# Kernel optimization log

Hardware: AMD Instinct MI355X
Metric: run time of the kernel (lower is better)

The kernel has to match this reference:

```python
import jax, jax.numpy as jnp
import numpy as np
from jax import lax

NPOINT = 1024   # num_points (FPS centroids)
RADIUS = 0.2    # ball-query radius
K = 32          # samples per ball
FILTERS = [64, 64, 128]


def setup_inputs() -> dict:
    key = jax.random.key(0)
    ks = jax.random.split(key, 10)
    B, N, C = 16, 4096, 64
    xyz = jax.random.uniform(ks[0], (B, N, 3), dtype=jnp.float32)   # unit-cube cloud
    points = jax.random.normal(ks[1], (B, N, C), dtype=jnp.float32)
    inp = {"xyz": xyz, "points": points}
    cin = C + 3  # use_xyz=True concatenates relative xyz
    for i, f in enumerate(FILTERS):
        scale = np.sqrt(2.0 / (cin + f)).astype(np.float32)  # glorot_normal
        inp[f"w{i}"] = jax.random.normal(ks[2 + i], (cin, f), dtype=jnp.float32) * scale
        inp[f"b{i}"] = jnp.zeros((f,), dtype=jnp.float32)
        cin = f
    return inp


def farthest_point_sample(xyz, npoint):
    # Serial greedy FPS. xyz: [B,N,3] -> idx [B,npoint] int32
    B, N, _ = xyz.shape

    def body(carry, _):
        dist, far = carry                                   # [B,N], [B]
        centroid = jnp.take_along_axis(xyz, far[:, None, None], axis=1)  # [B,1,3]
        d = jnp.sum((xyz - centroid) ** 2, axis=-1)         # [B,N]
        dist = jnp.minimum(dist, d)
        nxt = jnp.argmax(dist, axis=-1).astype(jnp.int32)
        return (dist, nxt), far

    init = (jnp.full((B, N), 1e10, xyz.dtype), jnp.zeros((B,), jnp.int32))
    _, idxs = lax.scan(body, init, None, length=npoint)
    return idxs.T  # [B,npoint]


def query_ball(radius, nsample, xyz, new_xyz):
    # First-nsample-in-order points within radius; pad with first hit (CUDA semantics).
    B, N, _ = xyz.shape
    d2 = jnp.sum((new_xyz[:, :, None, :] - xyz[:, None, :, :]) ** 2, axis=-1)  # [B,S,N]
    mask = d2 <= radius * radius
    order = jnp.where(mask, jnp.arange(N, dtype=jnp.int32)[None, None, :], N)
    idx_sorted = jnp.sort(order, axis=-1)[..., :nsample]    # first K valid indices
    first = idx_sorted[..., :1]
    first = jnp.where(first < N, first, 0)                  # empty-ball fallback
    return jnp.where(idx_sorted < N, idx_sorted, first)     # [B,S,K]


def reference(xyz, points, w0, b0, w1, b1, w2, b2):
    B, N, _ = xyz.shape
    fps_idx = farthest_point_sample(xyz, NPOINT)                    # [B,S]
    new_xyz = jnp.take_along_axis(xyz, fps_idx[:, :, None], axis=1)  # [B,S,3]
    idx = query_ball(RADIUS, K, xyz, new_xyz)                        # [B,S,K]

    bix = jnp.arange(B)[:, None, None]
    grouped_xyz = xyz[bix, idx] - new_xyz[:, :, None, :]             # [B,S,K,3] recentered
    grouped_pts = points[bix, idx]                                   # [B,S,K,C]
    g = jnp.concatenate([grouped_pts, grouped_xyz], axis=-1)         # [B,S,K,C+3]

    for w, b in ((w0, b0), (w1, b1), (w2, b2)):                      # shared 1x1-conv MLP
        g = jax.nn.relu(jnp.einsum('bskc,cf->bskf', g, w) + b)
    new_points = jnp.max(g, axis=2)                                  # max-pool over ball
    return new_xyz, new_points
```

## Files before the change

kernel.cpp:

```cpp
#include <hip/hip_runtime.h>
#include <stdint.h>

#define BB 16
#define NN 4096
#define CC 64
#define NPOINT 1024
#define KK 32
#define F1 64
#define F2 64
#define F3 128

#define FPS_T 512
#define PPT (NN / FPS_T)

#if defined(__has_builtin)
#if __has_builtin(__builtin_amdgcn_update_dpp)
#define HAS_DPP 1
#endif
#endif

#ifdef HAS_DPP
template <int CTRL>
__device__ __forceinline__ unsigned long long dpp_move64(unsigned long long k) {
    int lo = __builtin_amdgcn_update_dpp(0, (int)(unsigned)k,         CTRL, 0xF, 0xF, false);
    int hi = __builtin_amdgcn_update_dpp(0, (int)(unsigned)(k >> 32), CTRL, 0xF, 0xF, false);
    return ((unsigned long long)(unsigned)hi << 32) | (unsigned)lo;
}
__device__ __forceinline__ unsigned long long wave_max_key(unsigned long long key) {
    unsigned long long o;
    o = dpp_move64<0x111>(key); if (o > key) key = o;
    o = dpp_move64<0x112>(key); if (o > key) key = o;
    o = dpp_move64<0x114>(key); if (o > key) key = o;
    o = dpp_move64<0x118>(key); if (o > key) key = o;
    o = dpp_move64<0x142>(key); if (o > key) key = o;
    o = dpp_move64<0x143>(key); if (o > key) key = o;
    return key;
}
#else
__device__ __forceinline__ unsigned long long wave_max_key(unsigned long long key) {
#pragma unroll
    for (int off = 32; off > 0; off >>= 1) {
        unsigned long long o = __shfl_xor(key, off, 64);
        if (o > key) key = o;
    }
    return key;
}
#endif

#define SMEM_BYTES 83968

__global__ __launch_bounds__(512)
void fused_kernel(const float* __restrict__ xyz,
                  const float* __restrict__ points,
                  const float* __restrict__ w0, const float* __restrict__ b0,
                  const float* __restrict__ w1, const float* __restrict__ b1,
                  const float* __restrict__ w2, const float* __restrict__ b2,
                  float* __restrict__ out_xyz,
                  float* __restrict__ out_points,
                  int* __restrict__ ctr) {
    __shared__ __align__(16) char smem[SMEM_BYTES];
    const int tid = threadIdx.x;

    if (blockIdx.x < BB) {
        asm volatile("s_setprio 3");
        float* xs = (float*)smem;
        float* ys = xs + NN;
        float* zs = ys + NN;
        unsigned long long (*wred)[FPS_T / 64] =
            (unsigned long long (*)[FPS_T / 64])(smem + 49152);
        float* cbuf = (float*)(smem + 49280);

        const int b = blockIdx.x;
        const int lane = tid & 63, wid = tid >> 6;
        const float* __restrict__ xb = xyz + (size_t)b * (NN * 3);

        float px[PPT], py[PPT], pz[PPT], dist[PPT];
#pragma unroll
        for (int t = 0; t < PPT; ++t) {
            int p = tid + t * FPS_T;
            px[t] = xb[p * 3 + 0];
            py[t] = xb[p * 3 + 1];
            pz[t] = xb[p * 3 + 2];
            xs[p] = px[t]; ys[p] = py[t]; zs[p] = pz[t];
            dist[t] = 1e10f;
        }
        __syncthreads();

        float cx = xs[0], cy = ys[0], cz = zs[0];
        float* xo = out_xyz + (size_t)b * NPOINT * 3;

        for (int i = 0; i < NPOINT; ++i) {
            if (tid == 0) {
                cbuf[(i & 7) * 3 + 0] = cx;
                cbuf[(i & 7) * 3 + 1] = cy;
                cbuf[(i & 7) * 3 + 2] = cz;
            }
            float bd = -1.0f; int bp = 0;
#pragma unroll
            for (int t = 0; t < PPT; ++t) {
                float dx = __fsub_rn(px[t], cx);
                float dy = __fsub_rn(py[t], cy);
                float dz = __fsub_rn(pz[t], cz);
                float d  = __fadd_rn(__fadd_rn(__fmul_rn(dx, dx), __fmul_rn(dy, dy)),
                                     __fmul_rn(dz, dz));
                float nd = fminf(dist[t], d);
                dist[t] = nd;
                if (nd > bd) { bd = nd; bp = tid + t * FPS_T; }
            }
            unsigned long long key = (((unsigned long long)__float_as_uint(bd)) << 32)
                                   | (unsigned int)(NN - 1 - bp);
            key = wave_max_key(key);
            if (lane == 63) wred[i & 1][wid] = key;
            __syncthreads();

            unsigned long long best = wred[i & 1][0];
#pragma unroll
            for (int w = 1; w < FPS_T / 64; ++w) {
                unsigned long long o = wred[i & 1][w];
                if (o > best) best = o;
            }
            int bi = (NN - 1) - (int)(best & 0xffffffffu);

            cx = xs[bi]; cy = ys[bi]; cz = zs[bi];

            if (tid == 0 && (i & 7) == 7) {
                asm volatile("s_waitcnt vmcnt(0)" ::: "memory");
                if (i > 7)
                    __hip_atomic_store(&ctr[b * 16], i - 7,
                                       __ATOMIC_RELAXED, __HIP_MEMORY_SCOPE_AGENT);
                const unsigned* cbu = (const unsigned*)cbuf;
                unsigned* dst = (unsigned*)(xo + (size_t)(i - 7) * 3);
#pragma unroll
                for (int q = 0; q < 24; ++q)
                    __hip_atomic_store(dst + q, cbu[q],
                                       __ATOMIC_RELAXED, __HIP_MEMORY_SCOPE_AGENT);
            }
        }
        if (tid == 0) {
            asm volatile("s_waitcnt vmcnt(0)" ::: "memory");
            __hip_atomic_store(&ctr[b * 16], NPOINT,
                               __ATOMIC_RELAXED, __HIP_MEMORY_SCOPE_AGENT);
        }
    } else {
        float (*gbuf)[68] = (float (*)[68])smem;
        float (*hbuf)[F1] = (float (*)[F1])(smem + 8704);
        float (*pmax)[F3] = (float (*)[F3])(smem + 16896);
        unsigned long long* cmask = (unsigned long long*)(smem + 20992);
        int* nbr = (int*)(smem + 21504);

        const int gi = blockIdx.x - BB;
        const int s = gi >> 4;
        const int b = gi & 15;
        const int g = b * NPOINT + s;
        const int f = tid & 63;
        const int wid = tid >> 6;

        if (tid == 0) {
            while (__hip_atomic_load(&ctr[b * 16], __ATOMIC_RELAXED,
                                     __HIP_MEMORY_SCOPE_AGENT) < s + 1)
                __builtin_amdgcn_s_sleep(2);
        }
        __syncthreads();

        unsigned int ux = __hip_atomic_load((unsigned int*)&out_xyz[(size_t)g * 3 + 0],
                                            __ATOMIC_RELAXED, __HIP_MEMORY_SCOPE_AGENT);
        unsigned int uy = __hip_atomic_load((unsigned int*)&out_xyz[(size_t)g * 3 + 1],
                                            __ATOMIC_RELAXED, __HIP_MEMORY_SCOPE_AGENT);
        unsigned int uz = __hip_atomic_load((unsigned int*)&out_xyz[(size_t)g * 3 + 2],
                                            __ATOMIC_RELAXED, __HIP_MEMORY_SCOPE_AGENT);
        const float cx = __uint_as_float(ux);
        const float cy = __uint_as_float(uy);
        const float cz = __uint_as_float(uz);

        {
            const float* __restrict__ xb = xyz + (size_t)b * (NN * 3);
#pragma unroll
            for (int j = 0; j < 8; ++j) {
                int chunk = wid * 8 + j;
                int p = chunk * 64 + f;
                float x = xb[p * 3 + 0];
                float y = xb[p * 3 + 1];
                float z = xb[p * 3 + 2];
                float dx = __fsub_rn(cx, x);
                float dy = __fsub_rn(cy, y);
                float dz = __fsub_rn(cz, z);
                float d2 = __fadd_rn(__fadd_rn(__fmul_rn(dx, dx), __fmul_rn(dy, dy)),
                                     __fmul_rn(dz, dz));
                unsigned long long m = __ballot(d2 <= 0.04f);
                if (f == 0) cmask[chunk] = m;
            }
        }
        __syncthreads();

        if (tid < 64) {
            unsigned long long m = cmask[tid];
            int cnt = (int)__popcll(m);
            int v = cnt;
#pragma unroll
            for (int off = 1; off < 64; off <<= 1) {
                int u = __shfl_up(v, off, 64);
                if (tid >= off) v += u;
            }
            int excl = v - cnt;
            int total = __shfl(v, 63, 64);
            unsigned long long mm = m;
            int r = excl;
            while (mm && r < KK) {
                int bpos = __ffsll(mm) - 1;
                mm &= mm - 1;
                nbr[r++] = tid * 64 + bpos;
            }
            if (total < KK) {
                unsigned long long nz = __ballot(cnt > 0);
                int fchunk = __ffsll(nz) - 1;
                unsigned long long fm = cmask[fchunk];
                int first = fchunk * 64 + __ffsll(fm) - 1;
                if (tid >= total && tid < KK) nbr[tid] = first;
            }
        }
        __syncthreads();

        {
            const float* __restrict__ pb = points + (size_t)b * NN * CC;
#pragma unroll
            for (int m = 0; m < 4; ++m) {
                int k = wid + 8 * m;
                int idx = nbr[k] & (NN - 1);
                gbuf[k][f] = pb[(size_t)idx * CC + f];
            }
            if (tid < 96) {
                int k = tid & 31, q = tid >> 5;
                int idx = nbr[k] & (NN - 1);
                float v = xyz[((size_t)b * NN + idx) * 3 + q];
                float cq = (q == 0) ? cx : ((q == 1) ? cy : cz);
                gbuf[k][CC + q] = __fsub_rn(v, cq);
            }
        }
        __syncthreads();

        float acc[4];

#pragma unroll
        for (int m = 0; m < 4; ++m) acc[m] = 0.0f;
#pragma unroll 4
        for (int c4 = 0; c4 < 64; c4 += 4) {
            float wv0 = w0[(c4 + 0) * F1 + f];
            float wv1 = w0[(c4 + 1) * F1 + f];
            float wv2 = w0[(c4 + 2) * F1 + f];
            float wv3 = w0[(c4 + 3) * F1 + f];
#pragma unroll
            for (int m = 0; m < 4; ++m) {
                float4 gv = *(const float4*)&gbuf[wid + 8 * m][c4];
                acc[m] = fmaf(gv.x, wv0, acc[m]);
                acc[m] = fmaf(gv.y, wv1, acc[m]);
                acc[m] = fmaf(gv.z, wv2, acc[m]);
                acc[m] = fmaf(gv.w, wv3, acc[m]);
            }
        }
        {
            float wv0 = w0[64 * F1 + f];
            float wv1 = w0[65 * F1 + f];
            float wv2 = w0[66 * F1 + f];
#pragma unroll
            for (int m = 0; m < 4; ++m) {
                int k = wid + 8 * m;
                acc[m] = fmaf(gbuf[k][64], wv0, acc[m]);
                acc[m] = fmaf(gbuf[k][65], wv1, acc[m]);
                acc[m] = fmaf(gbuf[k][66], wv2, acc[m]);
            }
        }
        {
            float bb = b0[f];
#pragma unroll
            for (int m = 0; m < 4; ++m)
                hbuf[wid + 8 * m][f] = fmaxf(acc[m] + bb, 0.0f);
        }
        __syncthreads();

#pragma unroll
        for (int m = 0; m < 4; ++m) acc[m] = 0.0f;
#pragma unroll 4
        for (int c4 = 0; c4 < 64; c4 += 4) {
            float wv0 = w1[(c4 + 0) * F2 + f];
            float wv1 = w1[(c4 + 1) * F2 + f];
            float wv2 = w1[(c4 + 2) * F2 + f];
            float wv3 = w1[(c4 + 3) * F2 + f];
#pragma unroll
            for (int m = 0; m < 4; ++m) {
                float4 gv = *(const float4*)&hbuf[wid + 8 * m][c4];
                acc[m] = fmaf(gv.x, wv0, acc[m]);
                acc[m] = fmaf(gv.y, wv1, acc[m]);
                acc[m] = fmaf(gv.z, wv2, acc[m]);
                acc[m] = fmaf(gv.w, wv3, acc[m]);
            }
        }
        {
            float bb = b1[f];
#pragma unroll
            for (int m = 0; m < 4; ++m)
                gbuf[wid + 8 * m][f] = fmaxf(acc[m] + bb, 0.0f);
        }
        __syncthreads();

        float a0[4], a1[4];
#pragma unroll
        for (int m = 0; m < 4; ++m) { a0[m] = 0.0f; a1[m] = 0.0f; }
#pragma unroll 2
        for (int c4 = 0; c4 < 64; c4 += 4) {
            float w00 = w2[(c4 + 0) * F3 + f], w10 = w2[(c4 + 0) * F3 + f + 64];
            float w01 = w2[(c4 + 1) * F3 + f], w11 = w2[(c4 + 1) * F3 + f + 64];
            float w02 = w2[(c4 + 2) * F3 + f], w12 = w2[(c4 + 2) * F3 + f + 64];
            float w03 = w2[(c4 + 3) * F3 + f], w13 = w2[(c4 + 3) * F3 + f + 64];
#pragma unroll
            for (int m = 0; m < 4; ++m) {
                float4 gv = *(const float4*)&gbuf[wid + 8 * m][c4];
                a0[m] = fmaf(gv.x, w00, a0[m]);  a1[m] = fmaf(gv.x, w10, a1[m]);
                a0[m] = fmaf(gv.y, w01, a0[m]);  a1[m] = fmaf(gv.y, w11, a1[m]);
                a0[m] = fmaf(gv.z, w02, a0[m]);  a1[m] = fmaf(gv.z, w12, a1[m]);
                a0[m] = fmaf(gv.w, w03, a0[m]);  a1[m] = fmaf(gv.w, w13, a1[m]);
            }
        }
        {
            float pm0 = -1e30f, pm1 = -1e30f;
#pragma unroll
            for (int m = 0; m < 4; ++m) {
                pm0 = fmaxf(pm0, a0[m]);
                pm1 = fmaxf(pm1, a1[m]);
            }
            pmax[wid][f] = pm0;
            pmax[wid][f + 64] = pm1;
        }
        __syncthreads();
        if (tid < F3) {
            float v = pmax[0][tid];
#pragma unroll
            for (int w = 1; w < 8; ++w) v = fmaxf(v, pmax[w][tid]);
            v = fmaxf(v + b2[tid], 0.0f);
            out_points[(size_t)g * F3 + tid] = v;
        }
    }
}

extern "C" void kernel_launch(void* const* d_in, const int* in_sizes, int n_in,
                              void* d_out, int out_size, void* d_ws, size_t ws_size,
                              hipStream_t stream) {
    const float* xyz    = (const float*)d_in[0];
    const float* points = (const float*)d_in[1];
    const float* w0 = (const float*)d_in[2];
    const float* b0 = (const float*)d_in[3];
    const float* w1 = (const float*)d_in[4];
    const float* b1 = (const float*)d_in[5];
    const float* w2 = (const float*)d_in[6];
    const float* b2 = (const float*)d_in[7];

    float* out_xyz    = (float*)d_out;
    float* out_points = out_xyz + (size_t)BB * NPOINT * 3;
    int*   ctr        = (int*)d_ws;

    fused_kernel<<<BB + BB * NPOINT, 512, 0, stream>>>(
        xyz, points, w0, b0, w1, b1, w2, b2, out_xyz, out_points, ctr);
}
```

Measured before the change: 870.0 us.

## Process eight centroids per consumer block with xyz staged in shared memory

```diff
diff --git a/kernel.cpp b/kernel.cpp
--- a/kernel.cpp
+++ b/kernel.cpp
@@ -12,6 +12,7 @@
 
 #define FPS_T 512
 #define PPT (NN / FPS_T)
+#define GRP 8
 
 #if defined(__has_builtin)
 #if __has_builtin(__builtin_amdgcn_update_dpp)
@@ -47,7 +48,7 @@
 }
 #endif
 
-#define SMEM_BYTES 83968
+#define SMEM_BYTES 70784
 
 __global__ __launch_bounds__(512)
 void fused_kernel(const float* __restrict__ xyz,
@@ -61,11 +62,12 @@
     __shared__ __align__(16) char smem[SMEM_BYTES];
     const int tid = threadIdx.x;
 
+    float* xs = (float*)smem;
+    float* ys = xs + NN;
+    float* zs = ys + NN;
+
     if (blockIdx.x < BB) {
         asm volatile("s_setprio 3");
-        float* xs = (float*)smem;
-        float* ys = xs + NN;
-        float* zs = ys + NN;
         unsigned long long (*wred)[FPS_T / 64] =
             (unsigned long long (*)[FPS_T / 64])(smem + 49152);
         float* cbuf = (float*)(smem + 49280);
@@ -142,45 +144,63 @@
                                __ATOMIC_RELAXED, __HIP_MEMORY_SCOPE_AGENT);
         }
     } else {
-        float (*gbuf)[68] = (float (*)[68])smem;
-        float (*hbuf)[F1] = (float (*)[F1])(smem + 8704);
-        float (*pmax)[F3] = (float (*)[F3])(smem + 16896);
-        unsigned long long* cmask = (unsigned long long*)(smem + 20992);
-        int* nbr = (int*)(smem + 21504);
+        float (*gbuf)[68] = (float (*)[68])(smem + 49152);
+        float (*hbuf)[F1] = (float (*)[F1])(smem + 57856);
+        float (*pmax)[F3] = (float (*)[F3])(smem + 66048);
+        unsigned long long* cmask = (unsigned long long*)(smem + 70144);
+        int* nbr = (int*)(smem + 70656);
 
         const int gi = blockIdx.x - BB;
-        const int s = gi >> 4;
+        const int grp = gi >> 4;
         const int b = gi & 15;
-        const int g = b * NPOINT + s;
         const int f = tid & 63;
         const int wid = tid >> 6;
 
+        {
+            const float* __restrict__ xb = xyz + (size_t)b * (NN * 3);
+#pragma unroll
+            for (int t = 0; t < PPT; ++t) {
+                int p = tid + t * FPS_T;
+                xs[p] = xb[p * 3 + 0];
+                ys[p] = xb[p * 3 + 1];
+                zs[p] = xb[p * 3 + 2];
+            }
+        }
+
         if (tid == 0) {
             while (__hip_atomic_load(&ctr[b * 16], __ATOMIC_RELAXED,
-                                     __HIP_MEMORY_SCOPE_AGENT) < s + 1)
+                                     __HIP_MEMORY_SCOPE_AGENT) < GRP * grp + GRP)
                 __builtin_amdgcn_s_sleep(2);
         }
         __syncthreads();
 
-        unsigned int ux = __hip_atomic_load((unsigned int*)&out_xyz[(size_t)g * 3 + 0],
-                                            __ATOMIC_RELAXED, __HIP_MEMORY_SCOPE_AGENT);
-        unsigned int uy = __hip_atomic_load((unsigned int*)&out_xyz[(size_t)g * 3 + 1],
-                                            __ATOMIC_RELAXED, __HIP_MEMORY_SCOPE_AGENT);
-        unsigned int uz = __hip_atomic_load((unsigned int*)&out_xyz[(size_t)g * 3 + 2],
-                                            __ATOMIC_RELAXED, __HIP_MEMORY_SCOPE_AGENT);
-        const float cx = __uint_as_float(ux);
-        const float cy = __uint_as_float(uy);
-        const float cz = __uint_as_float(uz);
-
-        {
-            const float* __restrict__ xb = xyz + (size_t)b * (NN * 3);
+        float ccx[GRP], ccy[GRP], ccz[GRP];
+#pragma unroll
+        for (int ss = 0; ss < GRP; ++ss) {
+            size_t g3 = ((size_t)b * NPOINT + (size_t)grp * GRP + ss) * 3;
+            unsigned int ux = __hip_atomic_load((unsigned int*)&out_xyz[g3 + 0],
+                                                __ATOMIC_RELAXED, __HIP_MEMORY_SCOPE_AGENT);
+            unsigned int uy = __hip_atomic_load((unsigned int*)&out_xyz[g3 + 1],
+                                                __ATOMIC_RELAXED, __HIP_MEMORY_SCOPE_AGENT);
+            unsigned int uz = __hip_atomic_load((unsigned int*)&out_xyz[g3 + 2],
+                                                __ATOMIC_RELAXED, __HIP_MEMORY_SCOPE_AGENT);
+            ccx[ss] = __uint_as_float(ux);
+            ccy[ss] = __uint_as_float(uy);
+            ccz[ss] = __uint_as_float(uz);
+        }
+
+        for (int ss = 0; ss < GRP; ++ss) {
+            const int s = grp * GRP + ss;
+            const int g = b * NPOINT + s;
+            const float cx = ccx[ss], cy = ccy[ss], cz = ccz[ss];
+
 #pragma unroll
             for (int j = 0; j < 8; ++j) {
                 int chunk = wid * 8 + j;
                 int p = chunk * 64 + f;
-                float x = xb[p * 3 + 0];
-                float y = xb[p * 3 + 1];
-                float z = xb[p * 3 + 2];
+                float x = xs[p];
+                float y = ys[p];
+                float z = zs[p];
                 float dx = __fsub_rn(cx, x);
                 float dy = __fsub_rn(cy, y);
                 float dz = __fsub_rn(cz, z);
@@ -189,154 +209,155 @@
                 unsigned long long m = __ballot(d2 <= 0.04f);
                 if (f == 0) cmask[chunk] = m;
             }
-        }
-        __syncthreads();
-
-        if (tid < 64) {
-            unsigned long long m = cmask[tid];
-            int cnt = (int)__popcll(m);
-            int v = cnt;
-#pragma unroll
-            for (int off = 1; off < 64; off <<= 1) {
-                int u = __shfl_up(v, off, 64);
-                if (tid >= off) v += u;
-            }
-            int excl = v - cnt;
-            int total = __shfl(v, 63, 64);
-            unsigned long long mm = m;
-            int r = excl;
-            while (mm && r < KK) {
-                int bpos = __ffsll(mm) - 1;
-                mm &= mm - 1;
-                nbr[r++] = tid * 64 + bpos;
-            }
-            if (total < KK) {
-                unsigned long long nz = __ballot(cnt > 0);
-                int fchunk = __ffsll(nz) - 1;
-                unsigned long long fm = cmask[fchunk];
-                int first = fchunk * 64 + __ffsll(fm) - 1;
-                if (tid >= total && tid < KK) nbr[tid] = first;
-            }
-        }
-        __syncthreads();
-
-        {
-            const float* __restrict__ pb = points + (size_t)b * NN * CC;
-#pragma unroll
-            for (int m = 0; m < 4; ++m) {
-                int k = wid + 8 * m;
-                int idx = nbr[k] & (NN - 1);
-                gbuf[k][f] = pb[(size_t)idx * CC + f];
-            }
-            if (tid < 96) {
-                int k = tid & 31, q = tid >> 5;
-                int idx = nbr[k] & (NN - 1);
-                float v = xyz[((size_t)b * NN + idx) * 3 + q];
-                float cq = (q == 0) ? cx : ((q == 1) ? cy : cz);
-                gbuf[k][CC + q] = __fsub_rn(v, cq);
-            }
-        }
-        __syncthreads();
-
-        float acc[4];
-
-#pragma unroll
-        for (int m = 0; m < 4; ++m) acc[m] = 0.0f;
+            __syncthreads();
+
+            if (tid < 64) {
+                unsigned long long m = cmask[tid];
+                int cnt = (int)__popcll(m);
+                int v = cnt;
+#pragma unroll
+                for (int off = 1; off < 64; off <<= 1) {
+                    int u = __shfl_up(v, off, 64);
+                    if (tid >= off) v += u;
+                }
+                int excl = v - cnt;
+                int total = __shfl(v, 63, 64);
+                unsigned long long mm = m;
+                int r = excl;
+                while (mm && r < KK) {
+                    int bpos = __ffsll(mm) - 1;
+                    mm &= mm - 1;
+                    nbr[r++] = tid * 64 + bpos;
+                }
+                if (total < KK) {
+                    unsigned long long nz = __ballot(cnt > 0);
+                    int fchunk = __ffsll(nz) - 1;
+                    unsigned long long fm = cmask[fchunk];
+                    int first = fchunk * 64 + __ffsll(fm) - 1;
+                    if (tid >= total && tid < KK) nbr[tid] = first;
+                }
+            }
+            __syncthreads();
+
+            {
+                const float* __restrict__ pb = points + (size_t)b * NN * CC;
+#pragma unroll
+                for (int m = 0; m < 4; ++m) {
+                    int k = wid + 8 * m;
+                    int idx = nbr[k] & (NN - 1);
+                    gbuf[k][f] = pb[(size_t)idx * CC + f];
+                }
+                if (tid < 96) {
+                    int k = tid & 31, q = tid >> 5;
+                    int idx = nbr[k] & (NN - 1);
+                    float v = (q == 0) ? xs[idx] : ((q == 1) ? ys[idx] : zs[idx]);
+                    float cq = (q == 0) ? cx : ((q == 1) ? cy : cz);
+                    gbuf[k][CC + q] = __fsub_rn(v, cq);
+                }
+            }
+            __syncthreads();
+
+            float acc[4];
+
+#pragma unroll
+            for (int m = 0; m < 4; ++m) acc[m] = 0.0f;
 #pragma unroll 4
-        for (int c4 = 0; c4 < 64; c4 += 4) {
-            float wv0 = w0[(c4 + 0) * F1 + f];
-            float wv1 = w0[(c4 + 1) * F1 + f];
-            float wv2 = w0[(c4 + 2) * F1 + f];
-            float wv3 = w0[(c4 + 3) * F1 + f];
-#pragma unroll
-            for (int m = 0; m < 4; ++m) {
-                float4 gv = *(const float4*)&gbuf[wid + 8 * m][c4];
-                acc[m] = fmaf(gv.x, wv0, acc[m]);
-                acc[m] = fmaf(gv.y, wv1, acc[m]);
-                acc[m] = fmaf(gv.z, wv2, acc[m]);
-                acc[m] = fmaf(gv.w, wv3, acc[m]);
-            }
-        }
-        {
-            float wv0 = w0[64 * F1 + f];
-            float wv1 = w0[65 * F1 + f];
-            float wv2 = w0[66 * F1 + f];
-#pragma unroll
-            for (int m = 0; m < 4; ++m) {
-                int k = wid + 8 * m;
-                acc[m] = fmaf(gbuf[k][64], wv0, acc[m]);
-                acc[m] = fmaf(gbuf[k][65], wv1, acc[m]);
-                acc[m] = fmaf(gbuf[k][66], wv2, acc[m]);
-            }
-        }
-        {
-            float bb = b0[f];
-#pragma unroll
-            for (int m = 0; m < 4; ++m)
-                hbuf[wid + 8 * m][f] = fmaxf(acc[m] + bb, 0.0f);
-        }
-        __syncthreads();
-
-#pragma unroll
-        for (int m = 0; m < 4; ++m) acc[m] = 0.0f;
+            for (int c4 = 0; c4 < 64; c4 += 4) {
+                float wv0 = w0[(c4 + 0) * F1 + f];
+                float wv1 = w0[(c4 + 1) * F1 + f];
+                float wv2 = w0[(c4 + 2) * F1 + f];
+                float wv3 = w0[(c4 + 3) * F1 + f];
+#pragma unroll
+                for (int m = 0; m < 4; ++m) {
+                    float4 gv = *(const float4*)&gbuf[wid + 8 * m][c4];
+                    acc[m] = fmaf(gv.x, wv0, acc[m]);
+                    acc[m] = fmaf(gv.y, wv1, acc[m]);
+                    acc[m] = fmaf(gv.z, wv2, acc[m]);
+                    acc[m] = fmaf(gv.w, wv3, acc[m]);
+                }
+            }
+            {
+                float wv0 = w0[64 * F1 + f];
+                float wv1 = w0[65 * F1 + f];
+                float wv2 = w0[66 * F1 + f];
+#pragma unroll
+                for (int m = 0; m < 4; ++m) {
+                    int k = wid + 8 * m;
+                    acc[m] = fmaf(gbuf[k][64], wv0, acc[m]);
+                    acc[m] = fmaf(gbuf[k][65], wv1, acc[m]);
+                    acc[m] = fmaf(gbuf[k][66], wv2, acc[m]);
+                }
+            }
+            {
+                float bb = b0[f];
+#pragma unroll
+                for (int m = 0; m < 4; ++m)
+                    hbuf[wid + 8 * m][f] = fmaxf(acc[m] + bb, 0.0f);
+            }
+            __syncthreads();
+
+#pragma unroll
+            for (int m = 0; m < 4; ++m) acc[m] = 0.0f;
 #pragma unroll 4
-        for (int c4 = 0; c4 < 64; c4 += 4) {
-            float wv0 = w1[(c4 + 0) * F2 + f];
-            float wv1 = w1[(c4 + 1) * F2 + f];
-            float wv2 = w1[(c4 + 2) * F2 + f];
-            float wv3 = w1[(c4 + 3) * F2 + f];
-#pragma unroll
-            for (int m = 0; m < 4; ++m) {
-                float4 gv = *(const float4*)&hbuf[wid + 8 * m][c4];
-                acc[m] = fmaf(gv.x, wv0, acc[m]);
-                acc[m] = fmaf(gv.y, wv1, acc[m]);
-                acc[m] = fmaf(gv.z, wv2, acc[m]);
-                acc[m] = fmaf(gv.w, wv3, acc[m]);
-            }
-        }
-        {
-            float bb = b1[f];
-#pragma unroll
-            for (int m = 0; m < 4; ++m)
-                gbuf[wid + 8 * m][f] = fmaxf(acc[m] + bb, 0.0f);
-        }
-        __syncthreads();
-
-        float a0[4], a1[4];
-#pragma unroll
-        for (int m = 0; m < 4; ++m) { a0[m] = 0.0f; a1[m] = 0.0f; }
+            for (int c4 = 0; c4 < 64; c4 += 4) {
+                float wv0 = w1[(c4 + 0) * F2 + f];
+                float wv1 = w1[(c4 + 1) * F2 + f];
+                float wv2 = w1[(c4 + 2) * F2 + f];
+                float wv3 = w1[(c4 + 3) * F2 + f];
+#pragma unroll
+                for (int m = 0; m < 4; ++m) {
+                    float4 gv = *(const float4*)&hbuf[wid + 8 * m][c4];
+                    acc[m] = fmaf(gv.x, wv0, acc[m]);
+                    acc[m] = fmaf(gv.y, wv1, acc[m]);
+                    acc[m] = fmaf(gv.z, wv2, acc[m]);
+                    acc[m] = fmaf(gv.w, wv3, acc[m]);
+                }
+            }
+            {
+                float bb = b1[f];
+#pragma unroll
+                for (int m = 0; m < 4; ++m)
+                    gbuf[wid + 8 * m][f] = fmaxf(acc[m] + bb, 0.0f);
+            }
+            __syncthreads();
+
+            float a0[4], a1[4];
+#pragma unroll
+            for (int m = 0; m < 4; ++m) { a0[m] = 0.0f; a1[m] = 0.0f; }
 #pragma unroll 2
-        for (int c4 = 0; c4 < 64; c4 += 4) {
-            float w00 = w2[(c4 + 0) * F3 + f], w10 = w2[(c4 + 0) * F3 + f + 64];
-            float w01 = w2[(c4 + 1) * F3 + f], w11 = w2[(c4 + 1) * F3 + f + 64];
-            float w02 = w2[(c4 + 2) * F3 + f], w12 = w2[(c4 + 2) * F3 + f + 64];
-            float w03 = w2[(c4 + 3) * F3 + f], w13 = w2[(c4 + 3) * F3 + f + 64];
-#pragma unroll
-            for (int m = 0; m < 4; ++m) {
-                float4 gv = *(const float4*)&gbuf[wid + 8 * m][c4];
-                a0[m] = fmaf(gv.x, w00, a0[m]);  a1[m] = fmaf(gv.x, w10, a1[m]);
-                a0[m] = fmaf(gv.y, w01, a0[m]);  a1[m] = fmaf(gv.y, w11, a1[m]);
-                a0[m] = fmaf(gv.z, w02, a0[m]);  a1[m] = fmaf(gv.z, w12, a1[m]);
-                a0[m] = fmaf(gv.w, w03, a0[m]);  a1[m] = fmaf(gv.w, w13, a1[m]);
-            }
-        }
-        {
-            float pm0 = -1e30f, pm1 = -1e30f;
-#pragma unroll
-            for (int m = 0; m < 4; ++m) {
-                pm0 = fmaxf(pm0, a0[m]);
-                pm1 = fmaxf(pm1, a1[m]);
-            }
-            pmax[wid][f] = pm0;
-            pmax[wid][f + 64] = pm1;
-        }
-        __syncthreads();
-        if (tid < F3) {
-            float v = pmax[0][tid];
-#pragma unroll
-            for (int w = 1; w < 8; ++w) v = fmaxf(v, pmax[w][tid]);
-            v = fmaxf(v + b2[tid], 0.0f);
-            out_points[(size_t)g * F3 + tid] = v;
+            for (int c4 = 0; c4 < 64; c4 += 4) {
+                float w00 = w2[(c4 + 0) * F3 + f], w10 = w2[(c4 + 0) * F3 + f + 64];
+                float w01 = w2[(c4 + 1) * F3 + f], w11 = w2[(c4 + 1) * F3 + f + 64];
+                float w02 = w2[(c4 + 2) * F3 + f], w12 = w2[(c4 + 2) * F3 + f + 64];
+                float w03 = w2[(c4 + 3) * F3 + f], w13 = w2[(c4 + 3) * F3 + f + 64];
+#pragma unroll
+                for (int m = 0; m < 4; ++m) {
+                    float4 gv = *(const float4*)&gbuf[wid + 8 * m][c4];
+                    a0[m] = fmaf(gv.x, w00, a0[m]);  a1[m] = fmaf(gv.x, w10, a1[m]);
+                    a0[m] = fmaf(gv.y, w01, a0[m]);  a1[m] = fmaf(gv.y, w11, a1[m]);
+                    a0[m] = fmaf(gv.z, w02, a0[m]);  a1[m] = fmaf(gv.z, w12, a1[m]);
+                    a0[m] = fmaf(gv.w, w03, a0[m]);  a1[m] = fmaf(gv.w, w13, a1[m]);
+                }
+            }
+            {
+                float pm0 = -1e30f, pm1 = -1e30f;
+#pragma unroll
+                for (int m = 0; m < 4; ++m) {
+                    pm0 = fmaxf(pm0, a0[m]);
+                    pm1 = fmaxf(pm1, a1[m]);
+                }
+                pmax[wid][f] = pm0;
+                pmax[wid][f + 64] = pm1;
+            }
+            __syncthreads();
+            if (tid < F3) {
+                float v = pmax[0][tid];
+#pragma unroll
+                for (int w = 1; w < 8; ++w) v = fmaxf(v, pmax[w][tid]);
+                v = fmaxf(v + b2[tid], 0.0f);
+                out_points[(size_t)g * F3 + tid] = v;
+            }
+            __syncthreads();
         }
     }
 }
@@ -357,6 +378,6 @@
     float* out_points = out_xyz + (size_t)BB * NPOINT * 3;
     int*   ctr        = (int*)d_ws;
 
-    fused_kernel<<<BB + BB * NPOINT, 512, 0, stream>>>(
+    fused_kernel<<<BB + BB * (NPOINT / GRP), 512, 0, stream>>>(
         xyz, points, w0, b0, w1, b1, w2, b2, out_xyz, out_points, ctr);
 }
```

New measurement: 945.0 us. 1.09x slower.
